# Performance work log

Measured on AMD Instinct MI355X. Metric: run time of the kernel, lower is better.

Reference implementation:

```python
import jax, jax.numpy as jnp
import numpy as np

B, N, D = 4, 2048, 1024
H = 16
HD = D // H  # head_dim = 64
SCALE = HD ** -0.5


def setup_inputs() -> dict:
    key = jax.random.key(0)
    k1, k2, k3, k4 = jax.random.split(key, 4)
    x = jax.random.normal(k1, (B, N, D), dtype=jnp.float32)
    # init-scale weights for numerically sane softmax logits
    w_qkv = jax.random.normal(k2, (3 * D, D), dtype=jnp.float32) * 0.02
    w_proj = jax.random.normal(k3, (D, D), dtype=jnp.float32) * 0.02
    b_proj = jax.random.normal(k4, (D,), dtype=jnp.float32) * 0.02
    return {"x": x, "w_qkv": w_qkv, "w_proj": w_proj, "b_proj": b_proj}


def reference(x, w_qkv, w_proj, b_proj):
    # qkv projection (width_mult=1.0 -> Dyna slicing is identity; qkv_bias=False)
    qkv = jnp.einsum('bnd,ed->bne', x, w_qkv)          # (B, N, 3D)
    qkv = qkv.reshape(B, N, 3, H, HD)
    q = qkv[:, :, 0].transpose(0, 2, 1, 3)              # (B, H, N, HD)
    k = qkv[:, :, 1].transpose(0, 2, 1, 3)
    v = qkv[:, :, 2].transpose(0, 2, 1, 3)
    q = q * SCALE
    attn = jnp.einsum('bhqd,bhkd->bhqk', q, k)          # (B, H, N, N)
    attn = jax.nn.softmax(attn, axis=-1)
    out = jnp.einsum('bhqk,bhkd->bhqd', attn, v)        # (B, H, N, HD)
    out = out.transpose(0, 2, 1, 3).reshape(B, N, D)
    # output projection (bias=True)
    return jnp.einsum('bnd,ed->bne', out, w_proj) + b_proj
```

## Files before the change

kernel.cpp:

```cpp
#include <hip/hip_runtime.h>
#include <hip/hip_bf16.h>
#include <stdint.h>


typedef __attribute__((ext_vector_type(8))) short short8;
typedef __attribute__((ext_vector_type(4))) short short4v;
typedef __attribute__((ext_vector_type(4))) float float4v;

#define MFMA16(a, b, c) __builtin_amdgcn_mfma_f32_16x16x32_bf16((a), (b), (c), 0, 0, 0)
#define MFMA16K16(a, b, c) __builtin_amdgcn_mfma_f32_16x16x16bf16_1k((a), (b), (c), 0, 0, 0)

static __device__ __forceinline__ unsigned short f2bf(float f) {
  union { float f; unsigned u; } v; v.f = f;
  unsigned r = v.u + 0x7fffu + ((v.u >> 16) & 1u);
  return (unsigned short)(r >> 16);
}
static __device__ __forceinline__ float bf2f(unsigned short u) {
  union { unsigned u; float f; } v; v.u = ((unsigned)u) << 16;
  return v.f;
}
static __device__ __forceinline__ unsigned pkbf(float a, float b) {
  union { __hip_bfloat162 v; unsigned u; } c;
  c.v = __float22bfloat162_rn(make_float2(a, b));
  return c.u;
}
static __device__ __forceinline__ float4v fzero() {
  float4v z; z[0] = 0.f; z[1] = 0.f; z[2] = 0.f; z[3] = 0.f; return z;
}
static __device__ __forceinline__ void load_lds16(const void* g, void* l) {
  typedef const __attribute__((address_space(1))) void* gp_t;
  typedef __attribute__((address_space(3))) void* lp_t;
  __builtin_amdgcn_global_load_lds((gp_t)(uintptr_t)g, (lp_t)(uint32_t)(uintptr_t)l, 16, 0, 0);
}

__global__ void detect_dtype(const unsigned short* __restrict__ x, int* flag) {
  __shared__ int cnt;
  if (threadIdx.x == 0) cnt = 0;
  __syncthreads();
  int c = 0;
  for (int i = threadIdx.x; i < 4096; i += 256) {
    const unsigned v = x[i] & 0x7FFFu;
    if ((v >> 7) >= 134u) ++c;
  }
  atomicAdd(&cnt, c);
  __syncthreads();
  if (threadIdx.x == 0) *flag = (cnt > 64) ? 1 : 0;
}

static __device__ __forceinline__ void cv8(const void* src, unsigned short* dst,
                                           int i, int fl) {
  if (fl) {
    const float* s = (const float*)src + i;
    short8 o;
    for (int j = 0; j < 8; ++j) o[j] = (short)f2bf(s[j]);
    *(short8*)(dst + i) = o;
  } else {
    *(short8*)(dst + i) = *(const short8*)((const unsigned short*)src + i);
  }
}
__global__ __launch_bounds__(256) void convert_all(
    const void* __restrict__ s0, const void* __restrict__ s1,
    const void* __restrict__ s2, const void* __restrict__ s3,
    unsigned short* __restrict__ d0, unsigned short* __restrict__ d1,
    unsigned short* __restrict__ d2, unsigned short* __restrict__ d3,
    const int* __restrict__ flag) {
  const int t = blockIdx.x * 256 + threadIdx.x;
  const int fl = *flag;
  if (t < 1048576)       cv8(s0, d0, t * 8, fl);
  else if (t < 1441792)  cv8(s1, d1, (t - 1048576) * 8, fl);
  else if (t < 1572864)  cv8(s2, d2, (t - 1441792) * 8, fl);
  else if (t < 1572992)  cv8(s3, d3, (t - 1572864) * 8, fl);
}

__global__ __launch_bounds__(256) void qkv_gemm(
    const unsigned short* __restrict__ X, const unsigned short* __restrict__ W,
    unsigned short* __restrict__ Qo, unsigned short* __restrict__ Ko,
    unsigned short* __restrict__ Vt) {
  __shared__ __attribute__((aligned(16))) unsigned short lA[128 * 32];
  __shared__ __attribute__((aligned(16))) unsigned short lB[128 * 32];
  const int tid = threadIdx.x;
  const int wave = tid >> 6, lane = tid & 63, quad = lane >> 4, l16 = lane & 15;
  const int wm = wave >> 1, wn = wave & 1;
  const int m0 = blockIdx.x * 128, n0 = blockIdx.y * 128;

  float4v acc[4][4];
  for (int i = 0; i < 4; ++i) for (int j = 0; j < 4; ++j) acc[i][j] = fzero();

  const int f0 = tid, f1 = 256 + tid;
  const int r0 = f0 >> 2, c0 = (f0 & 3) * 8;
  const int r1 = f1 >> 2, c1 = (f1 & 3) * 8;
  unsigned short* dA0 = lA + (wave * 64) * 8;
  unsigned short* dA1 = lA + (256 + wave * 64) * 8;
  unsigned short* dB0 = lB + (wave * 64) * 8;
  unsigned short* dB1 = lB + (256 + wave * 64) * 8;

  for (int k0 = 0; k0 < 1024; k0 += 32) {
    __syncthreads();
    load_lds16(X + (size_t)(m0 + r0) * 1024 + k0 + c0, dA0);
    load_lds16(X + (size_t)(m0 + r1) * 1024 + k0 + c1, dA1);
    load_lds16(W + (size_t)(n0 + r0) * 1024 + k0 + c0, dB0);
    load_lds16(W + (size_t)(n0 + r1) * 1024 + k0 + c1, dB1);
    __syncthreads();
    short8 af[4], bfr[4];
    for (int t = 0; t < 4; ++t) {
      af[t]  = *(const short8*)(lA + (wm * 64 + t * 16 + l16) * 32 + quad * 8);
      bfr[t] = *(const short8*)(lB + (wn * 64 + t * 16 + l16) * 32 + quad * 8);
    }
    for (int mt = 0; mt < 4; ++mt)
      for (int nt = 0; nt < 4; ++nt)
        acc[mt][nt] = MFMA16(af[mt], bfr[nt], acc[mt][nt]);
  }

  for (int mt = 0; mt < 4; ++mt) {
    const int mbase = m0 + wm * 64 + mt * 16 + quad * 4;
    const int b = mbase >> 11;
    const int nrow = mbase & 2047;
    for (int nt = 0; nt < 4; ++nt) {
      const int e = n0 + wn * 64 + nt * 16 + l16;
      const int c = e >> 10, h = (e >> 6) & 15, hd = e & 63;
      const int bh = b * 16 + h;
      if (c == 0) {
        for (int r = 0; r < 4; ++r)
          Qo[((size_t)bh * 2048 + nrow + r) * 64 + hd] = f2bf(acc[mt][nt][r] * 0.125f);
      } else if (c == 1) {
        for (int r = 0; r < 4; ++r)
          Ko[((size_t)bh * 2048 + nrow + r) * 64 + hd] = f2bf(acc[mt][nt][r]);
      } else {
        short4v pk;
        for (int r = 0; r < 4; ++r) pk[r] = (short)f2bf(acc[mt][nt][r]);
        *(short4v*)(Vt + ((size_t)bh * 64 + hd) * 2048 + nrow) = pk;
      }
    }
  }
}

__global__ __launch_bounds__(256, 4) void flash_attn(
    const unsigned short* __restrict__ Q, const unsigned short* __restrict__ K,
    const unsigned short* __restrict__ Vt, unsigned short* __restrict__ AO) {
  __shared__ __attribute__((aligned(16))) unsigned short lK[64 * 72];
  __shared__ __attribute__((aligned(16))) unsigned short lV[64 * 72];
  const int tid = threadIdx.x;
  const int wave = tid >> 6, lane = tid & 63, quad = lane >> 4, l16 = lane & 15;
  const int qt = blockIdx.x, bh = blockIdx.y;
  const int b = bh >> 4, h = bh & 15;
  const size_t base = (size_t)bh * 2048 * 64;
  const unsigned short* Qp = Q + base;
  const unsigned short* Kp = K + base;
  const unsigned short* Vp = Vt + base;
  const int q0 = qt * 128;

  const int qa = q0 + wave * 16 + l16;
  const short8 qfA0 = *(const short8*)(Qp + (size_t)qa * 64 + quad * 8);
  const short8 qfA1 = *(const short8*)(Qp + (size_t)qa * 64 + 32 + quad * 8);
  const short8 qfB0 = *(const short8*)(Qp + (size_t)(qa + 64) * 64 + quad * 8);
  const short8 qfB1 = *(const short8*)(Qp + (size_t)(qa + 64) * 64 + 32 + quad * 8);

  float4v oaccA[4], oaccB[4];
  for (int i = 0; i < 4; ++i) { oaccA[i] = fzero(); oaccB[i] = fzero(); }
  float lsumA = 0.f, lsumB = 0.f;

  const int f0 = tid, f1 = 256 + tid;
  const int sk0 = (f0 >> 3) * 72 + (f0 & 7) * 8;
  const int sk1 = (f1 >> 3) * 72 + (f1 & 7) * 8;

  for (int kb = 0; kb < 32; ++kb) {
    const short8 kv0 = *(const short8*)(Kp + (size_t)kb * 4096 + f0 * 8);
    const short8 kv1 = *(const short8*)(Kp + (size_t)kb * 4096 + f1 * 8);
    const short8 vv0 = *(const short8*)(Vp + (size_t)(f0 >> 3) * 2048 + kb * 64 + (f0 & 7) * 8);
    const short8 vv1 = *(const short8*)(Vp + (size_t)(f1 >> 3) * 2048 + kb * 64 + (f1 & 7) * 8);
    __syncthreads();
    *(short8*)(lK + sk0) = kv0;
    *(short8*)(lK + sk1) = kv1;
    *(short8*)(lV + sk0) = vv0;
    *(short8*)(lV + sk1) = vv1;
    __syncthreads();

    float4v sA[4], sB[4];
    for (int t = 0; t < 4; ++t) {
      const short8 k0f = *(const short8*)(lK + (t * 16 + l16) * 72 + quad * 8);
      const short8 k1f = *(const short8*)(lK + (t * 16 + l16) * 72 + 32 + quad * 8);
      sA[t] = MFMA16(k0f, qfA0, fzero());
      sA[t] = MFMA16(k1f, qfA1, sA[t]);
      sB[t] = MFMA16(k0f, qfB0, fzero());
      sB[t] = MFMA16(k1f, qfB1, sB[t]);
    }

    short4v pA[4], pB[4];
    for (int t = 0; t < 4; ++t) {
      float eA0 = __expf(sA[t][0]), eA1 = __expf(sA[t][1]);
      float eA2 = __expf(sA[t][2]), eA3 = __expf(sA[t][3]);
      float eB0 = __expf(sB[t][0]), eB1 = __expf(sB[t][1]);
      float eB2 = __expf(sB[t][2]), eB3 = __expf(sB[t][3]);
      lsumA += (eA0 + eA1) + (eA2 + eA3);
      lsumB += (eB0 + eB1) + (eB2 + eB3);
      union { unsigned u[2]; short4v s; } ca, cb;
      ca.u[0] = pkbf(eA0, eA1); ca.u[1] = pkbf(eA2, eA3);
      cb.u[0] = pkbf(eB0, eB1); cb.u[1] = pkbf(eB2, eB3);
      pA[t] = ca.s; pB[t] = cb.s;
    }

    for (int nt = 0; nt < 4; ++nt) {
      const unsigned short* vrow = lV + (nt * 16 + l16) * 72 + quad * 4;
      for (int t = 0; t < 4; ++t) {
        const short4v vf = *(const short4v*)(vrow + t * 16);
        oaccA[nt] = MFMA16K16(vf, pA[t], oaccA[nt]);
        oaccB[nt] = MFMA16K16(vf, pB[t], oaccB[nt]);
      }
    }
  }

  lsumA += __shfl_xor(lsumA, 16); lsumA += __shfl_xor(lsumA, 32);
  lsumB += __shfl_xor(lsumB, 16); lsumB += __shfl_xor(lsumB, 32);
  const float invA = 1.f / lsumA, invB = 1.f / lsumB;

  unsigned short* aoA = AO + ((size_t)(b * 2048 + qa)) * 1024 + h * 64 + quad * 4;
  unsigned short* aoB = aoA + (size_t)64 * 1024;
  for (int nt = 0; nt < 4; ++nt) {
    union { unsigned u[2]; short4v s; } oa, ob;
    oa.u[0] = pkbf(oaccA[nt][0] * invA, oaccA[nt][1] * invA);
    oa.u[1] = pkbf(oaccA[nt][2] * invA, oaccA[nt][3] * invA);
    ob.u[0] = pkbf(oaccB[nt][0] * invB, oaccB[nt][1] * invB);
    ob.u[1] = pkbf(oaccB[nt][2] * invB, oaccB[nt][3] * invB);
    *(short4v*)(aoA + nt * 16) = oa.s;
    *(short4v*)(aoB + nt * 16) = ob.s;
  }
}

__global__ __launch_bounds__(256) void proj_gemm(
    const unsigned short* __restrict__ A, const unsigned short* __restrict__ W,
    const unsigned short* __restrict__ bias_bf, const void* __restrict__ bias_raw,
    void* __restrict__ outv, const int* __restrict__ flag) {
  __shared__ __attribute__((aligned(16))) unsigned short lA[128 * 32];
  __shared__ __attribute__((aligned(16))) unsigned short lB[128 * 32];
  const int tid = threadIdx.x;
  const int wave = tid >> 6, lane = tid & 63, quad = lane >> 4, l16 = lane & 15;
  const int wm = wave >> 1, wn = wave & 1;
  const int m0 = blockIdx.x * 128, n0 = blockIdx.y * 128;
  const int fl = *flag;

  float4v acc[4][4];
  for (int i = 0; i < 4; ++i) for (int j = 0; j < 4; ++j) acc[i][j] = fzero();

  const int f0 = tid, f1 = 256 + tid;
  const int r0 = f0 >> 2, c0 = (f0 & 3) * 8;
  const int r1 = f1 >> 2, c1 = (f1 & 3) * 8;
  unsigned short* dA0 = lA + (wave * 64) * 8;
  unsigned short* dA1 = lA + (256 + wave * 64) * 8;
  unsigned short* dB0 = lB + (wave * 64) * 8;
  unsigned short* dB1 = lB + (256 + wave * 64) * 8;

  for (int k0 = 0; k0 < 1024; k0 += 32) {
    __syncthreads();
    load_lds16(A + (size_t)(m0 + r0) * 1024 + k0 + c0, dA0);
    load_lds16(A + (size_t)(m0 + r1) * 1024 + k0 + c1, dA1);
    load_lds16(W + (size_t)(n0 + r0) * 1024 + k0 + c0, dB0);
    load_lds16(W + (size_t)(n0 + r1) * 1024 + k0 + c1, dB1);
    __syncthreads();
    short8 af[4], bfr[4];
    for (int t = 0; t < 4; ++t) {
      af[t]  = *(const short8*)(lA + (wm * 64 + t * 16 + l16) * 32 + quad * 8);
      bfr[t] = *(const short8*)(lB + (wn * 64 + t * 16 + l16) * 32 + quad * 8);
    }
    for (int mt = 0; mt < 4; ++mt)
      for (int nt = 0; nt < 4; ++nt)
        acc[mt][nt] = MFMA16(af[mt], bfr[nt], acc[mt][nt]);
  }

  for (int mt = 0; mt < 4; ++mt) {
    const int mbase = m0 + wm * 64 + mt * 16 + quad * 4;
    for (int nt = 0; nt < 4; ++nt) {
      const int e = n0 + wn * 64 + nt * 16 + l16;
      const float bv = fl ? ((const float*)bias_raw)[e] : bf2f(bias_bf[e]);
      for (int r = 0; r < 4; ++r) {
        const float val = acc[mt][nt][r] + bv;
        const size_t idx = (size_t)(mbase + r) * 1024 + e;
        if (fl) ((float*)outv)[idx] = val;
        else    ((unsigned short*)outv)[idx] = f2bf(val);
      }
    }
  }
}

extern "C" void kernel_launch(void* const* d_in, const int* in_sizes, int n_in,
                              void* d_out, int out_size, void* d_ws, size_t ws_size,
                              hipStream_t stream) {
  const void* x_raw     = d_in[0];
  const void* wqkv_raw  = d_in[1];
  const void* wproj_raw = d_in[2];
  const void* bproj_raw = d_in[3];

  const size_t NE = (size_t)4 * 16 * 2048 * 64;
  unsigned short* ws = (unsigned short*)d_ws;
  unsigned short* Q      = ws;
  unsigned short* K      = Q + NE;
  unsigned short* Vt     = K + NE;
  unsigned short* xb     = Vt + NE;
  unsigned short* AO     = xb;
  unsigned short* wqkvb  = xb + NE;
  unsigned short* wprojb = wqkvb + 3145728;
  unsigned short* bprojb = wprojb + 1048576;
  int* flag = (int*)(bprojb + 1024);

  detect_dtype<<<1, 256, 0, stream>>>((const unsigned short*)x_raw, flag);
  convert_all<<<6145, 256, 0, stream>>>(x_raw, wqkv_raw, wproj_raw, bproj_raw,
                                        xb, wqkvb, wprojb, bprojb, flag);

  qkv_gemm<<<dim3(64, 24), 256, 0, stream>>>(xb, wqkvb, Q, K, Vt);
  flash_attn<<<dim3(16, 64), 256, 0, stream>>>(Q, K, Vt, AO);
  proj_gemm<<<dim3(64, 8), 256, 0, stream>>>(AO, wprojb, bprojb, bproj_raw,
                                             d_out, flag);
}
```

Baseline: 300.3 us.

## Double-buffer K/V tiles, prefetch next block, and use exp2 with folded log2e scale

The attention loop now uses two LDS buffers for K and V and issues the global loads for the next key block right after the barrier, so they overlap the current block's MFMA work. This drops one barrier per iteration. The Q scale now folds in log2(e), so the softmax can use the hardware exp2 instruction instead of __expf. The QK, exp and PV steps are also interleaved per 16-key subtile to cut register pressure, at the cost of twice the LDS per block, which may reduce occupancy.

Measured after the change: 285.8 us. -4.8%, faster.

```diff
diff --git a/kernel.cpp b/kernel.cpp
--- a/kernel.cpp
+++ b/kernel.cpp
@@ -23,6 +23,13 @@
   union { __hip_bfloat162 v; unsigned u; } c;
   c.v = __float22bfloat162_rn(make_float2(a, b));
   return c.u;
+}
+static __device__ __forceinline__ float ex2(float x) {
+#if __has_builtin(__builtin_amdgcn_exp2f)
+  return __builtin_amdgcn_exp2f(x);
+#else
+  return exp2f(x);
+#endif
 }
 static __device__ __forceinline__ float4v fzero() {
   float4v z; z[0] = 0.f; z[1] = 0.f; z[2] = 0.f; z[3] = 0.f; return z;
@@ -111,6 +118,7 @@
         acc[mt][nt] = MFMA16(af[mt], bfr[nt], acc[mt][nt]);
   }
 
+  const float QSCALE = 0.18033688011112042f;
   for (int mt = 0; mt < 4; ++mt) {
     const int mbase = m0 + wm * 64 + mt * 16 + quad * 4;
     const int b = mbase >> 11;
@@ -121,7 +129,7 @@
       const int bh = b * 16 + h;
       if (c == 0) {
         for (int r = 0; r < 4; ++r)
-          Qo[((size_t)bh * 2048 + nrow + r) * 64 + hd] = f2bf(acc[mt][nt][r] * 0.125f);
+          Qo[((size_t)bh * 2048 + nrow + r) * 64 + hd] = f2bf(acc[mt][nt][r] * QSCALE);
       } else if (c == 1) {
         for (int r = 0; r < 4; ++r)
           Ko[((size_t)bh * 2048 + nrow + r) * 64 + hd] = f2bf(acc[mt][nt][r]);
@@ -137,8 +145,8 @@
 __global__ __launch_bounds__(256, 4) void flash_attn(
     const unsigned short* __restrict__ Q, const unsigned short* __restrict__ K,
     const unsigned short* __restrict__ Vt, unsigned short* __restrict__ AO) {
-  __shared__ __attribute__((aligned(16))) unsigned short lK[64 * 72];
-  __shared__ __attribute__((aligned(16))) unsigned short lV[64 * 72];
+  __shared__ __attribute__((aligned(16))) unsigned short lK[2][64 * 72];
+  __shared__ __attribute__((aligned(16))) unsigned short lV[2][64 * 72];
   const int tid = threadIdx.x;
   const int wave = tid >> 6, lane = tid & 63, quad = lane >> 4, l16 = lane & 15;
   const int qt = blockIdx.x, bh = blockIdx.y;
@@ -163,48 +171,52 @@
   const int sk0 = (f0 >> 3) * 72 + (f0 & 7) * 8;
   const int sk1 = (f1 >> 3) * 72 + (f1 & 7) * 8;
 
+  short8 kv0 = *(const short8*)(Kp + f0 * 8);
+  short8 kv1 = *(const short8*)(Kp + f1 * 8);
+  short8 vv0 = *(const short8*)(Vp + (size_t)(f0 >> 3) * 2048 + (f0 & 7) * 8);
+  short8 vv1 = *(const short8*)(Vp + (size_t)(f1 >> 3) * 2048 + (f1 & 7) * 8);
+
   for (int kb = 0; kb < 32; ++kb) {
-    const short8 kv0 = *(const short8*)(Kp + (size_t)kb * 4096 + f0 * 8);
-    const short8 kv1 = *(const short8*)(Kp + (size_t)kb * 4096 + f1 * 8);
-    const short8 vv0 = *(const short8*)(Vp + (size_t)(f0 >> 3) * 2048 + kb * 64 + (f0 & 7) * 8);
-    const short8 vv1 = *(const short8*)(Vp + (size_t)(f1 >> 3) * 2048 + kb * 64 + (f1 & 7) * 8);
-    __syncthreads();
-    *(short8*)(lK + sk0) = kv0;
-    *(short8*)(lK + sk1) = kv1;
-    *(short8*)(lV + sk0) = vv0;
-    *(short8*)(lV + sk1) = vv1;
-    __syncthreads();
-
-    float4v sA[4], sB[4];
+    unsigned short* const Kb = lK[kb & 1];
+    unsigned short* const Vb = lV[kb & 1];
+    *(short8*)(Kb + sk0) = kv0;
+    *(short8*)(Kb + sk1) = kv1;
+    *(short8*)(Vb + sk0) = vv0;
+    *(short8*)(Vb + sk1) = vv1;
+    __syncthreads();
+    if (kb < 31) {
+      const size_t ko = (size_t)(kb + 1) * 4096;
+      kv0 = *(const short8*)(Kp + ko + f0 * 8);
+      kv1 = *(const short8*)(Kp + ko + f1 * 8);
+      vv0 = *(const short8*)(Vp + (size_t)(f0 >> 3) * 2048 + (kb + 1) * 64 + (f0 & 7) * 8);
+      vv1 = *(const short8*)(Vp + (size_t)(f1 >> 3) * 2048 + (kb + 1) * 64 + (f1 & 7) * 8);
+    }
+
+#pragma unroll
     for (int t = 0; t < 4; ++t) {
-      const short8 k0f = *(const short8*)(lK + (t * 16 + l16) * 72 + quad * 8);
-      const short8 k1f = *(const short8*)(lK + (t * 16 + l16) * 72 + 32 + quad * 8);
-      sA[t] = MFMA16(k0f, qfA0, fzero());
-      sA[t] = MFMA16(k1f, qfA1, sA[t]);
-      sB[t] = MFMA16(k0f, qfB0, fzero());
-      sB[t] = MFMA16(k1f, qfB1, sB[t]);
-    }
-
-    short4v pA[4], pB[4];
-    for (int t = 0; t < 4; ++t) {
-      float eA0 = __expf(sA[t][0]), eA1 = __expf(sA[t][1]);
-      float eA2 = __expf(sA[t][2]), eA3 = __expf(sA[t][3]);
-      float eB0 = __expf(sB[t][0]), eB1 = __expf(sB[t][1]);
-      float eB2 = __expf(sB[t][2]), eB3 = __expf(sB[t][3]);
+      const short8 k0f = *(const short8*)(Kb + (t * 16 + l16) * 72 + quad * 8);
+      const short8 k1f = *(const short8*)(Kb + (t * 16 + l16) * 72 + 32 + quad * 8);
+      float4v sA = MFMA16(k0f, qfA0, fzero());
+      sA = MFMA16(k1f, qfA1, sA);
+      float4v sB = MFMA16(k0f, qfB0, fzero());
+      sB = MFMA16(k1f, qfB1, sB);
+
+      const float eA0 = ex2(sA[0]), eA1 = ex2(sA[1]);
+      const float eA2 = ex2(sA[2]), eA3 = ex2(sA[3]);
+      const float eB0 = ex2(sB[0]), eB1 = ex2(sB[1]);
+      const float eB2 = ex2(sB[2]), eB3 = ex2(sB[3]);
       lsumA += (eA0 + eA1) + (eA2 + eA3);
       lsumB += (eB0 + eB1) + (eB2 + eB3);
       union { unsigned u[2]; short4v s; } ca, cb;
       ca.u[0] = pkbf(eA0, eA1); ca.u[1] = pkbf(eA2, eA3);
       cb.u[0] = pkbf(eB0, eB1); cb.u[1] = pkbf(eB2, eB3);
-      pA[t] = ca.s; pB[t] = cb.s;
-    }
-
-    for (int nt = 0; nt < 4; ++nt) {
-      const unsigned short* vrow = lV + (nt * 16 + l16) * 72 + quad * 4;
-      for (int t = 0; t < 4; ++t) {
-        const short4v vf = *(const short4v*)(vrow + t * 16);
-        oaccA[nt] = MFMA16K16(vf, pA[t], oaccA[nt]);
-        oaccB[nt] = MFMA16K16(vf, pB[t], oaccB[nt]);
+
+      const unsigned short* vrow = Vb + l16 * 72 + quad * 4 + t * 16;
+#pragma unroll
+      for (int nt = 0; nt < 4; ++nt) {
+        const short4v vf = *(const short4v*)(vrow + nt * 16 * 72);
+        oaccA[nt] = MFMA16K16(vf, ca.s, oaccA[nt]);
+        oaccB[nt] = MFMA16K16(vf, cb.s, oaccB[nt]);
       }
     }
   }
```
